# Kernel tuning notes

Measured on AMD Instinct MI355X. Metric: run time of the kernel, lower is better.

The kernel has to match this reference:

```python
import jax, jax.numpy as jnp
import numpy as np
from jax import lax

GAMMA = 1.0

def _conv(x, w, b, stride, pad):
    y = lax.conv_general_dilated(x, w, (stride, stride), [(pad, pad), (pad, pad)],
                                 dimension_numbers=('NCHW', 'OIHW', 'NCHW'))
    return y + b[None, :, None, None]

def _maxpool2s1(x):
    return lax.reduce_window(x, -jnp.inf, lax.max, (1, 1, 2, 2), (1, 1, 1, 1), 'VALID')

def setup_inputs() -> dict:
    key = jax.random.key(0)
    ks = jax.random.split(key, 13)
    d = {}
    d['x'] = jax.random.normal(ks[0], (128, 3, 250, 250), dtype=jnp.float32)
    d['conv1_w'] = jax.random.normal(ks[1], (6, 3, 5, 5), dtype=jnp.float32) / np.sqrt(3 * 25)
    d['conv1_b'] = jax.random.normal(ks[2], (6,), dtype=jnp.float32) * 0.01
    d['conv2_w'] = jax.random.normal(ks[3], (15, 6, 3, 3), dtype=jnp.float32) / np.sqrt(6 * 9)
    d['conv2_b'] = jax.random.normal(ks[4], (15,), dtype=jnp.float32) * 0.01
    d['fc1_w'] = jax.random.normal(ks[5], (120, 55815), dtype=jnp.float32) / np.sqrt(55815.0)
    d['fc1_b'] = jax.random.normal(ks[6], (120,), dtype=jnp.float32) * 0.01
    d['fc2_w'] = jax.random.normal(ks[7], (84, 120), dtype=jnp.float32) / np.sqrt(120.0)
    d['fc2_b'] = jax.random.normal(ks[8], (84,), dtype=jnp.float32) * 0.01
    d['fc3_w'] = jax.random.normal(ks[9], (1, 84), dtype=jnp.float32) / np.sqrt(84.0)
    d['fc3_b'] = jax.random.normal(ks[10], (1,), dtype=jnp.float32) * 0.01
    d['support'] = jax.random.normal(ks[11], (10, 1), dtype=jnp.float32)
    return d

def reference(x, conv1_w, conv1_b, conv2_w, conv2_b, fc1_w, fc1_b, fc2_w, fc2_b, fc3_w, fc3_b, support):
    h = jax.nn.relu(_conv(x, conv1_w, conv1_b, 2, 1))   # [B,6,124,124]
    h = _maxpool2s1(h)                                   # [B,6,123,123] (dropout = identity in eval)
    h = jax.nn.relu(_conv(h, conv2_w, conv2_b, 2, 1))    # [B,15,62,62]
    h = _maxpool2s1(h)                                   # [B,15,61,61]
    h = h.reshape(h.shape[0], -1)                        # [B,55815]
    h = jax.nn.relu(h @ fc1_w.T + fc1_b)
    h = jax.nn.relu(h @ fc2_w.T + fc2_b)
    h = h @ fc3_w.T + fc3_b                              # [B,1]
    # fused RBF kernel vs support set: k[i,j] = exp(-gamma*(x_i - s_j)^2)
    diff = h - support[:, 0][None, :]                    # [B,10]
    k = jnp.exp(-GAMMA * diff * diff)
    h = k.mean(axis=1, keepdims=True)                    # [B,1]
    probs = jax.nn.sigmoid(h)
    return jnp.concatenate((probs, 1.0 - probs), axis=-1)  # [B,2]
```

## Files before the change

kernel.cpp:

```cpp
#include <hip/hip_runtime.h>
#include <math.h>


#define BATCH 128
#define KPAD 55816

#define C1_ST 78
#define C1_COLS 69
#define C1_ROWS 67
#define C1_TOT (C1_ROWS * C1_COLS)
__global__ __launch_bounds__(256) void conv1_pool_kernel(
    const float* __restrict__ x, const float* __restrict__ w,
    const float* __restrict__ bias, float* __restrict__ out) {
  const int b = blockIdx.z;
  const int P0 = blockIdx.x * 32;
  const int R0 = blockIdx.y * 31;
  const int tid = threadIdx.x;
  const int t = tid >> 3;
  const int s = tid & 7;

  __shared__ float lds[C1_ROWS * C1_ST];
  float* cbuf = lds;

  float acc[5][6];
#pragma unroll
  for (int oc = 0; oc < 6; oc++) {
    float bv = bias[oc];
#pragma unroll
    for (int dc = 0; dc < 5; dc++) acc[dc][oc] = bv;
  }

  const int ihb = 2 * R0 - 1, iwb = 2 * P0 - 1;

#pragma unroll 1
  for (int ci = 0; ci < 3; ci++) {
    __syncthreads();
    const float* src = x + (size_t)(b * 3 + ci) * 62500;
#pragma unroll 1
    for (int base = tid; base < C1_TOT; base += 1024) {
      float vv[4];
      int lrv[4], ilv[4];
#pragma unroll
      for (int k = 0; k < 4; k++) {
        int i = base + (k << 8);
        int lr = (int)(((unsigned)i * 121575u) >> 23);
        int il = i - lr * 69;
        lrv[k] = lr; ilv[k] = il;
        int ih = ihb + lr, iw = iwb + il;
        bool ok = (i < C1_TOT) && ((unsigned)ih < 250u) && ((unsigned)iw < 250u);
        vv[k] = ok ? src[ih * 250 + iw] : 0.f;
      }
#pragma unroll
      for (int k = 0; k < 4; k++) {
        int i = base + (k << 8);
        if (i < C1_TOT) lds[lrv[k] * C1_ST + ilv[k] + (ilv[k] >> 3)] = vv[k];
      }
    }
    __syncthreads();

    const float* rbase = &lds[(2 * t) * C1_ST + 9 * s];
#pragma unroll
    for (int ir = 0; ir < 5; ir++) {
      const float* rpl = rbase + ir * C1_ST;
      const float* rph = rpl + 1;
      float v[13];
#pragma unroll
      for (int j = 0; j < 8; j++)  v[j] = rpl[j];
#pragma unroll
      for (int j = 8; j < 13; j++) v[j] = rph[j];
#pragma unroll
      for (int oc = 0; oc < 6; oc++) {
        const float* wr = w + ((oc * 3 + ci) * 5 + ir) * 5;
        float w0 = wr[0], w1 = wr[1], w2 = wr[2], w3 = wr[3], w4 = wr[4];
#pragma unroll
        for (int dc = 0; dc < 5; dc++) {
          float a = acc[dc][oc];
          a += w0 * v[2 * dc + 0];
          a += w1 * v[2 * dc + 1];
          a += w2 * v[2 * dc + 2];
          a += w3 * v[2 * dc + 3];
          a += w4 * v[2 * dc + 4];
          acc[dc][oc] = a;
        }
      }
    }
  }

  __syncthreads();
  if (t == 8 || t == 16 || t == 24) {
    float* cb = &cbuf[(((t >> 3) - 1) * 8 + s) * 30];
#pragma unroll
    for (int oc = 0; oc < 6; oc++)
#pragma unroll
      for (int dc = 0; dc < 5; dc++) cb[oc * 5 + dc] = acc[dc][oc];
  }
  __syncthreads();

  const int p0 = R0 + t;
  const int c0 = P0 + 4 * s;
  const bool edge = ((t & 7) == 7) && (t < 31);
  const bool wr_ok = (t < 31) && (p0 < 123);
  const float* cb = &cbuf[((t >> 3) * 8 + s) * 30];

#pragma unroll
  for (int oc = 0; oc < 6; oc++) {
    float a0 = acc[0][oc], a1 = acc[1][oc], a2 = acc[2][oc],
          a3 = acc[3][oc], a4 = acc[4][oc];
    float n0 = __shfl_down(a0, 8), n1 = __shfl_down(a1, 8),
          n2 = __shfl_down(a2, 8), n3 = __shfl_down(a3, 8),
          n4 = __shfl_down(a4, 8);
    if (edge) {
      n0 = cb[oc * 5 + 0]; n1 = cb[oc * 5 + 1]; n2 = cb[oc * 5 + 2];
      n3 = cb[oc * 5 + 3]; n4 = cb[oc * 5 + 4];
    }
    if (wr_ok) {
      float* orow = out + ((size_t)(b * 6 + oc) * 123 + p0) * 123;
      float m0 = fmaxf(fmaxf(fmaxf(a0, a1), fmaxf(n0, n1)), 0.f);
      float m1 = fmaxf(fmaxf(fmaxf(a1, a2), fmaxf(n1, n2)), 0.f);
      float m2 = fmaxf(fmaxf(fmaxf(a2, a3), fmaxf(n2, n3)), 0.f);
      float m3 = fmaxf(fmaxf(fmaxf(a3, a4), fmaxf(n3, n4)), 0.f);
      if (c0 + 3 < 123) {
        *(float4*)&orow[c0] = make_float4(m0, m1, m2, m3);
      } else {
        if (c0 < 123) orow[c0] = m0;
        if (c0 + 1 < 123) orow[c0 + 1] = m1;
        if (c0 + 2 < 123) orow[c0 + 2] = m2;
      }
    }
  }
}

#define C2_ST 84
#define C2_TOT (35 * 67)
__global__ __launch_bounds__(256) void conv2_pool_kernel(
    const float* __restrict__ in, const float* __restrict__ w,
    const float* __restrict__ bias, float* __restrict__ out) {
  const int b = blockIdx.z;
  const int P0 = blockIdx.x * 32;
  const int R0 = blockIdx.y * 16;
  const int tid = threadIdx.x;
  const int t = tid >> 4;
  const int s = tid & 15;

  __shared__ float lds[35 * C2_ST];

  const int ihb = 2 * R0 - 1, iwb = 2 * P0 - 1;
  const int r = R0 + t;
  const int c0 = P0 + 2 * s;

  float acc0[3][15], acc1[3][15];
#pragma unroll
  for (int oc = 0; oc < 15; oc++) {
    float bv = bias[oc];
#pragma unroll
    for (int dc = 0; dc < 3; dc++) { acc0[dc][oc] = bv; acc1[dc][oc] = bv; }
  }

#pragma unroll 1
  for (int ci = 0; ci < 6; ci++) {
    __syncthreads();
    const float* src = in + (size_t)(b * 6 + ci) * 15129;
#pragma unroll 1
    for (int base = tid; base < C2_TOT; base += 1024) {
      float vv[4];
      int ladr[4];
#pragma unroll
      for (int k = 0; k < 4; k++) {
        int i = base + (k << 8);
        int lr = (int)(((unsigned)i * 125204u) >> 23);
        int il = i - lr * 67;
        int ih = ihb + lr, iw = iwb + il;
        bool ok = (i < C2_TOT) && ((unsigned)ih < 123u) && ((unsigned)iw < 123u);
        vv[k] = ok ? src[ih * 123 + iw] : 0.f;
        ladr[k] = (i < C2_TOT) ? (lr * C2_ST + il + (il >> 2)) : -1;
      }
#pragma unroll
      for (int k = 0; k < 4; k++) {
        if (ladr[k] >= 0) lds[ladr[k]] = vv[k];
      }
    }
    __syncthreads();

#pragma unroll 1
    for (int ir = 0; ir < 5; ir++) {
      const float* rp = &lds[(2 * t + ir) * C2_ST + 5 * s];
      float v[7];
#pragma unroll
      for (int j = 0; j < 7; j++) v[j] = rp[j + (j >> 2)];

      if (ir < 3) {
#pragma unroll
        for (int oc = 0; oc < 15; oc++) {
          const float* wr = w + ((oc * 6 + ci) * 3 + ir) * 3;
          float w0 = wr[0], w1 = wr[1], w2 = wr[2];
#pragma unroll
          for (int dc = 0; dc < 3; dc++) {
            float a = acc0[dc][oc];
            a += w0 * v[2 * dc + 0];
            a += w1 * v[2 * dc + 1];
            a += w2 * v[2 * dc + 2];
            acc0[dc][oc] = a;
          }
        }
      }
      if (ir >= 2) {
#pragma unroll
        for (int oc = 0; oc < 15; oc++) {
          const float* wr = w + ((oc * 6 + ci) * 3 + (ir - 2)) * 3;
          float w0 = wr[0], w1 = wr[1], w2 = wr[2];
#pragma unroll
          for (int dc = 0; dc < 3; dc++) {
            float a = acc1[dc][oc];
            a += w0 * v[2 * dc + 0];
            a += w1 * v[2 * dc + 1];
            a += w2 * v[2 * dc + 2];
            acc1[dc][oc] = a;
          }
        }
      }
    }
  }

  if (r < 61) {
#pragma unroll
    for (int oc = 0; oc < 15; oc++) {
      float* orow = out + (size_t)b * KPAD + (oc * 3721 + r * 61);
      float m0 = fmaxf(fmaxf(fmaxf(acc0[0][oc], acc0[1][oc]),
                             fmaxf(acc1[0][oc], acc1[1][oc])), 0.f);
      float m1 = fmaxf(fmaxf(fmaxf(acc0[1][oc], acc0[2][oc]),
                             fmaxf(acc1[1][oc], acc1[2][oc])), 0.f);
      if (c0 + 1 < 61) {
        *(float2*)&orow[c0] = make_float2(m0, m1);
      } else if (c0 < 61) {
        orow[c0] = m0;
      }
    }
  }
}

#define KTOT 55815
#define NPART 512
#define KCHUNK 112
#define KSTEP 16
__global__ __launch_bounds__(512) void fc1_splitk_kernel(
    const float* __restrict__ act, const float* __restrict__ w,
    float* __restrict__ partial) {
  const int kbase = blockIdx.x * KCHUNK;
  const int tid = threadIdx.x;
  const int tx = tid & 31, ty = tid >> 5;
  __shared__ float ldsA[KSTEP * 132];
  __shared__ float ldsB[KSTEP * 132];
  float acc[8][4];
#pragma unroll
  for (int i = 0; i < 8; i++)
#pragma unroll
    for (int j = 0; j < 4; j++) acc[i][j] = 0.f;

  const int mA = tid >> 2;
  const int qA = (tid & 3) * 4;

  for (int s16 = 0; s16 < KCHUNK / KSTEP; s16++) {
    int kofs = kbase + s16 * KSTEP;
    __syncthreads();
    {
      int k = kofs + qA;
      float4 a4;
      if (k + 3 < KTOT) {
        a4 = *(const float4*)&act[(size_t)mA * KPAD + k];
      } else {
        a4.x = (k + 0 < KTOT) ? act[(size_t)mA * KPAD + k + 0] : 0.f;
        a4.y = (k + 1 < KTOT) ? act[(size_t)mA * KPAD + k + 1] : 0.f;
        a4.z = (k + 2 < KTOT) ? act[(size_t)mA * KPAD + k + 2] : 0.f;
        a4.w = (k + 3 < KTOT) ? act[(size_t)mA * KPAD + k + 3] : 0.f;
      }
      ldsA[(qA + 0) * 132 + mA] = a4.x;
      ldsA[(qA + 1) * 132 + mA] = a4.y;
      ldsA[(qA + 2) * 132 + mA] = a4.z;
      ldsA[(qA + 3) * 132 + mA] = a4.w;
    }
    for (int i = tid; i < 1920; i += 512) {
      int n = i >> 4, kk = i & 15;
      int k = kofs + kk;
      ldsB[kk * 132 + n] = (k < KTOT) ? w[n * KTOT + k] : 0.f;
    }
    __syncthreads();
#pragma unroll
    for (int kk = 0; kk < KSTEP; kk++) {
      float4 a0 = *(const float4*)&ldsA[kk * 132 + ty * 8];
      float4 a1 = *(const float4*)&ldsA[kk * 132 + ty * 8 + 4];
      float4 b0 = *(const float4*)&ldsB[kk * 132 + tx * 4];
      float av[8] = {a0.x, a0.y, a0.z, a0.w, a1.x, a1.y, a1.z, a1.w};
      float bv[4] = {b0.x, b0.y, b0.z, b0.w};
#pragma unroll
      for (int i = 0; i < 8; i++)
#pragma unroll
        for (int j = 0; j < 4; j++) acc[i][j] += av[i] * bv[j];
    }
  }

  if (tx < 30) {
    float* dst = partial + (size_t)blockIdx.x * 15360;
#pragma unroll
    for (int i = 0; i < 8; i++) {
      int row = ty * 8 + i;
      float4 st = make_float4(acc[i][0], acc[i][1], acc[i][2], acc[i][3]);
      *(float4*)&dst[row * 120 + tx * 4] = st;
    }
  }
}

__global__ __launch_bounds__(256) void fc1_reduce_kernel(
    const float* __restrict__ partial, const float* __restrict__ bias,
    float* __restrict__ h1) {
  const int g = threadIdx.x >> 5, il = threadIdx.x & 31;
  const int idx = blockIdx.x * 32 + il;
  const float* p = partial + (size_t)g * 15360 + idx;
  float s = 0.f;
#pragma unroll 8
  for (int q = 0; q < 64; q++) s += p[(size_t)(q * 8) * 15360];
  __shared__ float red[8][32];
  red[g][il] = s;
  __syncthreads();
  if (threadIdx.x < 32) {
    float tsum = 0.f;
#pragma unroll
    for (int gg = 0; gg < 8; gg++) tsum += red[gg][threadIdx.x];
    h1[idx] = fmaxf(tsum + bias[idx % 120], 0.f);
  }
}

__global__ __launch_bounds__(128) void head_kernel(
    const float* __restrict__ h1, const float* __restrict__ fc2_w,
    const float* __restrict__ fc2_b, const float* __restrict__ fc3_w,
    const float* __restrict__ fc3_b, const float* __restrict__ support,
    float* __restrict__ out) {
  int b = blockIdx.x, t = threadIdx.x;
  __shared__ float hrow[120];
  __shared__ float s2[84];
  if (t < 120) hrow[t] = h1[b * 120 + t];
  __syncthreads();
  if (t < 84) {
    float d = fc2_b[t];
    for (int k = 0; k < 120; k++) d += fc2_w[t * 120 + k] * hrow[k];
    s2[t] = fmaxf(d, 0.f);
  }
  __syncthreads();
  if (t == 0) {
    float h = fc3_b[0];
    for (int j = 0; j < 84; j++) h += fc3_w[j] * s2[j];
    float ks = 0.f;
    for (int j = 0; j < 10; j++) {
      float diff = h - support[j];
      ks += expf(-diff * diff);
    }
    ks *= 0.1f;
    float p = 1.f / (1.f + expf(-ks));
    out[b * 2] = p;
    out[b * 2 + 1] = 1.f - p;
  }
}

extern "C" void kernel_launch(void* const* d_in, const int* in_sizes, int n_in,
                              void* d_out, int out_size, void* d_ws, size_t ws_size,
                              hipStream_t stream) {
  const float* x   = (const float*)d_in[0];
  const float* c1w = (const float*)d_in[1];
  const float* c1b = (const float*)d_in[2];
  const float* c2w = (const float*)d_in[3];
  const float* c2b = (const float*)d_in[4];
  const float* f1w = (const float*)d_in[5];
  const float* f1b = (const float*)d_in[6];
  const float* f2w = (const float*)d_in[7];
  const float* f2b = (const float*)d_in[8];
  const float* f3w = (const float*)d_in[9];
  const float* f3b = (const float*)d_in[10];
  const float* sup = (const float*)d_in[11];
  float* out = (float*)d_out;

  char* ws = (char*)d_ws;
  float* pool1 = (float*)ws;
  float* act   = (float*)(ws + 46476288);
  float* part  = (float*)ws;
  float* h1    = (float*)(ws + 33000000);

  conv1_pool_kernel<<<dim3(4, 4, BATCH), 256, 0, stream>>>(x, c1w, c1b, pool1);
  conv2_pool_kernel<<<dim3(2, 4, BATCH), 256, 0, stream>>>(pool1, c2w, c2b, act);
  fc1_splitk_kernel<<<NPART, 512, 0, stream>>>(act, f1w, part);
  fc1_reduce_kernel<<<480, 256, 0, stream>>>(part, f1b, h1);
  head_kernel<<<BATCH, 128, 0, stream>>>(h1, f2w, f2b, f3w, f3b, sup, out);
}
```

Baseline: 326.7 us.

## Share neighbor conv rows across threads instead of recomputing in conv2 pool

Each thread in the conv2+pool kernel previously computed two conv output rows, its own and the next one, so the 2x2 stride-1 pooling could run locally. Now each thread computes only its own row and gets the next row from the thread 16 lanes down via __shfl_down. Rows that cross a wavefront boundary are exchanged through LDS, and the last row of the tile is computed separately by the t==15 threads. This roughly halves conv FMAs at the cost of extra syncs, shuffles, and a divergent tail computation for the last row group.

```diff
diff --git a/kernel.cpp b/kernel.cpp
--- a/kernel.cpp
+++ b/kernel.cpp
@@ -143,12 +143,14 @@
   const int s = tid & 15;
 
   __shared__ float lds[35 * C2_ST];
+  float* cbuf = lds;
 
   const int ihb = 2 * R0 - 1, iwb = 2 * P0 - 1;
   const int r = R0 + t;
   const int c0 = P0 + 2 * s;
 
-  float acc0[3][15], acc1[3][15];
+  float acc0[3][15];
+  float acc1[3][15];
 #pragma unroll
   for (int oc = 0; oc < 15; oc++) {
     float bv = bias[oc];
@@ -182,31 +184,35 @@
     __syncthreads();
 
 #pragma unroll 1
-    for (int ir = 0; ir < 5; ir++) {
+    for (int ir = 0; ir < 3; ir++) {
       const float* rp = &lds[(2 * t + ir) * C2_ST + 5 * s];
       float v[7];
 #pragma unroll
       for (int j = 0; j < 7; j++) v[j] = rp[j + (j >> 2)];
-
-      if (ir < 3) {
+#pragma unroll
+      for (int oc = 0; oc < 15; oc++) {
+        const float* wr = w + ((oc * 6 + ci) * 3 + ir) * 3;
+        float w0 = wr[0], w1 = wr[1], w2 = wr[2];
+#pragma unroll
+        for (int dc = 0; dc < 3; dc++) {
+          float a = acc0[dc][oc];
+          a += w0 * v[2 * dc + 0];
+          a += w1 * v[2 * dc + 1];
+          a += w2 * v[2 * dc + 2];
+          acc0[dc][oc] = a;
+        }
+      }
+    }
+    if (t == 15) {
+#pragma unroll 1
+      for (int kh = 0; kh < 3; kh++) {
+        const float* rp = &lds[(32 + kh) * C2_ST + 5 * s];
+        float v[7];
+#pragma unroll
+        for (int j = 0; j < 7; j++) v[j] = rp[j + (j >> 2)];
 #pragma unroll
         for (int oc = 0; oc < 15; oc++) {
-          const float* wr = w + ((oc * 6 + ci) * 3 + ir) * 3;
-          float w0 = wr[0], w1 = wr[1], w2 = wr[2];
-#pragma unroll
-          for (int dc = 0; dc < 3; dc++) {
-            float a = acc0[dc][oc];
-            a += w0 * v[2 * dc + 0];
-            a += w1 * v[2 * dc + 1];
-            a += w2 * v[2 * dc + 2];
-            acc0[dc][oc] = a;
-          }
-        }
-      }
-      if (ir >= 2) {
-#pragma unroll
-        for (int oc = 0; oc < 15; oc++) {
-          const float* wr = w + ((oc * 6 + ci) * 3 + (ir - 2)) * 3;
+          const float* wr = w + ((oc * 6 + ci) * 3 + kh) * 3;
           float w0 = wr[0], w1 = wr[1], w2 = wr[2];
 #pragma unroll
           for (int dc = 0; dc < 3; dc++) {
@@ -221,14 +227,35 @@
     }
   }
 
-  if (r < 61) {
-#pragma unroll
-    for (int oc = 0; oc < 15; oc++) {
+  __syncthreads();
+  if (t == 4 || t == 8 || t == 12) {
+    float* cb = &cbuf[(((t >> 2) - 1) * 16 + s) * 45];
+#pragma unroll
+    for (int oc = 0; oc < 15; oc++)
+#pragma unroll
+      for (int dc = 0; dc < 3; dc++) cb[oc * 3 + dc] = acc0[dc][oc];
+  }
+  __syncthreads();
+
+  const bool edge = (t == 3 || t == 7 || t == 11);
+  const float* cb = &cbuf[((t >> 2) * 16 + s) * 45];
+  const bool wr_ok = (r < 61);
+
+#pragma unroll
+  for (int oc = 0; oc < 15; oc++) {
+    float a0 = acc0[0][oc], a1 = acc0[1][oc], a2 = acc0[2][oc];
+    float n0 = __shfl_down(a0, 16), n1 = __shfl_down(a1, 16),
+          n2 = __shfl_down(a2, 16);
+    if (edge) {
+      n0 = cb[oc * 3 + 0]; n1 = cb[oc * 3 + 1]; n2 = cb[oc * 3 + 2];
+    }
+    if (t == 15) {
+      n0 = acc1[0][oc]; n1 = acc1[1][oc]; n2 = acc1[2][oc];
+    }
+    if (wr_ok) {
       float* orow = out + (size_t)b * KPAD + (oc * 3721 + r * 61);
-      float m0 = fmaxf(fmaxf(fmaxf(acc0[0][oc], acc0[1][oc]),
-                             fmaxf(acc1[0][oc], acc1[1][oc])), 0.f);
-      float m1 = fmaxf(fmaxf(fmaxf(acc0[1][oc], acc0[2][oc]),
-                             fmaxf(acc1[1][oc], acc1[2][oc])), 0.f);
+      float m0 = fmaxf(fmaxf(fmaxf(a0, a1), fmaxf(n0, n1)), 0.f);
+      float m1 = fmaxf(fmaxf(fmaxf(a1, a2), fmaxf(n1, n2)), 0.f);
       if (c0 + 1 < 61) {
         *(float2*)&orow[c0] = make_float2(m0, m1);
       } else if (c0 < 61) {
```

Measured after the change: 320.0 us. 1.02x faster.
